# Kernel tuning notes

Hardware: AMD Instinct MI355X
Metric: run time of the kernel (lower is better)

The kernel has to match this reference:

```python
import jax, jax.numpy as jnp
import numpy as np

B, D, H = 8, 512, 8
HD = D // H            # 64 head dim
NS, NT = 8192, 4096    # search / template points
ATTN_EPS = 1e-6
LN_EPS = 1e-5


def layer_norm(x, g, b):
    m = jnp.mean(x, axis=-1, keepdims=True)
    v = jnp.mean((x - m) ** 2, axis=-1, keepdims=True)
    return (x - m) * jax.lax.rsqrt(v + LN_EPS) * g + b


def setup_inputs() -> dict:
    key = jax.random.key(0)
    ks = jax.random.split(key, 20)
    s = 0.02
    return {
        "search_feat": jax.random.normal(ks[0], (B, D, NS), jnp.float32),
        "search_xyz": jax.random.uniform(ks[1], (B, NS, 3), jnp.float32),
        "template_feat": jax.random.normal(ks[2], (B, D, NT), jnp.float32),
        "template_xyz": jax.random.uniform(ks[3], (B, NT, 3), jnp.float32),
        "pos_w1": jax.random.normal(ks[4], (3, D), jnp.float32) * s,
        "pos_b1": jnp.zeros((D,), jnp.float32),
        "pos_w2": jax.random.normal(ks[5], (D, D), jnp.float32) * s,
        "pos_b2": jnp.zeros((D,), jnp.float32),
        "wq": jax.random.normal(ks[6], (D, D), jnp.float32) * s,
        "wk": jax.random.normal(ks[7], (D, D), jnp.float32) * s,
        "wv": jax.random.normal(ks[8], (D, D), jnp.float32) * s,
        "w_merge": jax.random.normal(ks[9], (D, D), jnp.float32) * s,
        "mlp_w1": jax.random.normal(ks[10], (2 * D, 2 * D), jnp.float32) * s,
        "mlp_w2": jax.random.normal(ks[11], (2 * D, D), jnp.float32) * s,
        "ln1_g": jnp.ones((D,), jnp.float32),
        "ln1_b": jnp.zeros((D,), jnp.float32),
        "ln2_g": jnp.ones((D,), jnp.float32),
        "ln2_b": jnp.zeros((D,), jnp.float32),
    }


def reference(search_feat, search_xyz, template_feat, template_xyz,
              pos_w1, pos_b1, pos_w2, pos_b2, wq, wk, wv, w_merge,
              mlp_w1, mlp_w2, ln1_g, ln1_b, ln2_g, ln2_b):
    bs = search_feat.shape[0]
    sf = jnp.transpose(search_feat, (0, 2, 1))    # [B, Ns, D]
    tf = jnp.transpose(template_feat, (0, 2, 1))  # [B, Nt, D]

    # positional MLP on template coordinates
    pos = jax.nn.relu(template_xyz @ pos_w1 + pos_b1) @ pos_w2 + pos_b2
    tf_pos = tf + pos

    q = (sf @ wq).reshape(bs, NS, H, HD)
    k = (tf @ wk).reshape(bs, NT, H, HD)
    v = (tf_pos @ wv).reshape(bs, NT, H, HD)

    # LoFTR-style linear attention: phi(x) = elu(x) + 1
    Q = jax.nn.elu(q) + 1.0
    K = jax.nn.elu(k) + 1.0
    v_len = v.shape[1]
    v_n = v / v_len
    KV = jnp.einsum("bshd,bshv->bhdv", K, v_n)                 # [B,H,d,d]
    Z = 1.0 / (jnp.einsum("blhd,bhd->blh", Q, K.sum(axis=1)) + ATTN_EPS)
    msg = jnp.einsum("blhd,bhdv->blhv", Q, KV) * Z[..., None] * v_len

    msg = msg.reshape(bs, NS, H * HD) @ w_merge
    msg = layer_norm(msg, ln1_g, ln1_b)
    cat = jnp.concatenate([sf, msg], axis=2)                    # [B,Ns,2D]
    msg = jax.nn.relu(cat @ mlp_w1) @ mlp_w2
    msg = layer_norm(msg, ln2_g, ln2_b)
    return jnp.transpose(sf + msg, (0, 2, 1))                   # [B,D,Ns]
```

## Files before the change

kernel.cpp:

```cpp
#include <hip/hip_runtime.h>
#include <stdint.h>
#include <stddef.h>


using ushort_t = unsigned short;
using short8 = __attribute__((ext_vector_type(8))) short;
using f32x4  = __attribute__((ext_vector_type(4))) float;

#define DEVI __device__ __forceinline__

DEVI float b2f(unsigned short u) {
    unsigned v = ((unsigned)u) << 16;
    return __builtin_bit_cast(float, v);
}
DEVI unsigned short f2b(float x) {
    unsigned u = __builtin_bit_cast(unsigned, x);
    u += 0x7FFFu + ((u >> 16) & 1u);
    return (unsigned short)(u >> 16);
}
DEVI void gload16(const void* g, void* l) {
    __builtin_amdgcn_global_load_lds(
        (const __attribute__((address_space(1))) unsigned*)g,
        (__attribute__((address_space(3))) unsigned*)l, 16, 0, 0);
}

template <int EPI>
__global__ __launch_bounds__(512, 2)
void gemm_bf16(const ushort_t* __restrict__ A0, const ushort_t* __restrict__ A1,
               const ushort_t* __restrict__ Wt, ushort_t* __restrict__ C,
               const float* __restrict__ bias, const ushort_t* __restrict__ addm,
               int N, int K, int K0, int lda0, int lda1, int nn)
{
    __shared__ ushort_t As[2][256 * 64];
    __shared__ ushort_t Bs[2][256 * 64];
    const int tid = threadIdx.x;
    const int cpx = gridDim.x >> 3;
    const int lid = (blockIdx.x & 7) * cpx + (blockIdx.x >> 3);
    const int m0 = (lid / nn) * 256;
    const int n0 = (lid % nn) * 256;
    const int w = tid >> 6, l = tid & 63;
    const int wm = (w >> 2) * 128;
    const int wn = (w & 3) * 64;
    const int lr = l & 15, lg = l >> 4;
    const int srow = tid >> 3;
    const int sck  = (tid & 7) ^ (srow & 7);
    const int nk = K / 64;

    f32x4 accA[4][4] = {};
    f32x4 accB[4][4] = {};

    auto stageA = [&](int kt, int buf) {
        const int kb = kt * 64;
        const ushort_t* p; int ld;
        if (kb < K0) { p = A0 + (size_t)m0 * lda0 + kb; ld = lda0; }
        else         { p = A1 + (size_t)m0 * lda1 + (kb - K0); ld = lda1; }
        p += (size_t)srow * ld + sck * 8;
#pragma unroll
        for (int j = 0; j < 4; j++)
            gload16(p + (size_t)(j * 64) * ld,
                    (void*)(&As[buf][j * 4096] + tid * 8));
    };
    auto stageB = [&](int kt, int buf) {
        const ushort_t* p = Wt + (size_t)(n0 + srow) * K + kt * 64 + sck * 8;
#pragma unroll
        for (int j = 0; j < 4; j++)
            gload16(p + (size_t)(j * 64) * K,
                    (void*)(&Bs[buf][j * 4096] + tid * 8));
    };

    short8 aP[4], aQ[4], aR[4], b0[4], b1[4];

    auto ldA = [&](short8 (&dst)[4], int mh, int ks, int cb) {
#pragma unroll
        for (int mf = 0; mf < 4; mf++) {
            const int r = wm + mh * 64 + mf * 16 + lr;
            dst[mf] = *(const short8*)&As[cb][r * 64 + ((ks * 4 + lg) ^ (r & 7)) * 8];
        }
    };
    auto ldB = [&](short8 (&dst)[4], int ks, int cb) {
#pragma unroll
        for (int nf = 0; nf < 4; nf++) {
            const int r = wn + nf * 16 + lr;
            dst[nf] = *(const short8*)&Bs[cb][r * 64 + ((ks * 4 + lg) ^ (r & 7)) * 8];
        }
    };
    auto MM = [&](f32x4 (&ac)[4][4], short8 (&af)[4], short8 (&bf)[4]) {
        __builtin_amdgcn_s_setprio(1);
#pragma unroll
        for (int mf = 0; mf < 4; mf++)
#pragma unroll
            for (int nf = 0; nf < 4; nf++)
                ac[mf][nf] = __builtin_amdgcn_mfma_f32_16x16x32_bf16(
                    af[mf], bf[nf], ac[mf][nf], 0, 0, 0);
        __builtin_amdgcn_s_setprio(0);
    };

    stageA(0, 0); stageB(0, 0);
    asm volatile("s_waitcnt vmcnt(0)" ::: "memory");
    __builtin_amdgcn_s_barrier();
    ldA(aP, 0, 0, 0); ldB(b0, 0, 0);

    for (int t = 0; t < nk; ++t) {
        const int cur = t & 1;
        const bool pre = (t + 1) < nk;
        ldA(aQ, 1, 0, cur); ldB(b1, 1, cur);
        if (pre) stageA(t + 1, cur ^ 1);
        MM(accA, aP, b0);
        ldA(aR, 0, 1, cur);
        if (pre) stageB(t + 1, cur ^ 1);
        MM(accB, aQ, b0);
        ldA(aP, 1, 1, cur);
        MM(accA, aR, b1);
        MM(accB, aP, b1);
        if (pre) {
            asm volatile("s_waitcnt vmcnt(0)" ::: "memory");
            __builtin_amdgcn_s_barrier();
            ldA(aP, 0, 0, cur ^ 1); ldB(b0, 0, cur ^ 1);
        }
    }

#pragma unroll
    for (int mf = 0; mf < 4; mf++) {
#pragma unroll
        for (int i = 0; i < 4; i++) {
            const int mA = m0 + wm + mf * 16 + lg * 4 + i;
            const int mB = mA + 64;
#pragma unroll
            for (int nf = 0; nf < 4; nf++) {
                const int n = n0 + wn + nf * 16 + lr;
                float x = accA[mf][nf][i];
                float y = accB[mf][nf][i];
                if constexpr (EPI == 1) {
                    x = x > 0.f ? x + 1.f : __expf(x);
                    y = y > 0.f ? y + 1.f : __expf(y);
                }
                if constexpr (EPI == 2) {
                    x += bias[n] + b2f(addm[(size_t)mA * N + n]);
                    y += bias[n] + b2f(addm[(size_t)mB * N + n]);
                }
                if constexpr (EPI == 3) { x = fmaxf(x, 0.f); y = fmaxf(y, 0.f); }
                C[(size_t)mA * N + n] = f2b(x);
                C[(size_t)mB * N + n] = f2b(y);
            }
        }
    }
}

__global__ __launch_bounds__(256)
void transpose_f32_bf16(const float* __restrict__ in, ushort_t* __restrict__ out,
                        int R, int Cc)
{
    __shared__ float tile[64][65];
    const int t = threadIdx.x;
    const int c0 = blockIdx.x * 64, r0 = blockIdx.y * 64;
    const size_t bo = (size_t)blockIdx.z * (size_t)R * (size_t)Cc;
    const float* src = in + bo;
    ushort_t* dst = out + bo;
#pragma unroll
    for (int i = 0; i < 4; i++) {
        const int r = (t >> 4) + i * 16;
        const int c = (t & 15) * 4;
        const float4 v = *(const float4*)&src[(size_t)(r0 + r) * Cc + c0 + c];
        tile[r][c + 0] = v.x; tile[r][c + 1] = v.y;
        tile[r][c + 2] = v.z; tile[r][c + 3] = v.w;
    }
    __syncthreads();
#pragma unroll
    for (int i = 0; i < 2; i++) {
        const int c = (t >> 3) + i * 32;
        const int rs = (t & 7) * 8;
        short8 o;
#pragma unroll
        for (int j = 0; j < 8; j++) o[j] = (short)f2b(tile[rs + j][c]);
        *(short8*)&dst[(size_t)(c0 + c) * R + r0 + rs] = o;
    }
}

__global__ __launch_bounds__(256)
void pos_mlp1(const float* __restrict__ xyz, const float* __restrict__ w1,
              const float* __restrict__ b1, ushort_t* __restrict__ P1)
{
    const int t = threadIdx.x;
    const int m = blockIdx.x * 4 + (t >> 6);
    const int n0 = (t & 63) * 8;
    const float x = xyz[m * 3 + 0], y = xyz[m * 3 + 1], z = xyz[m * 3 + 2];
    short8 o;
#pragma unroll
    for (int j = 0; j < 8; j++) {
        const int n = n0 + j;
        float v = x * w1[n] + y * w1[512 + n] + z * w1[1024 + n] + b1[n];
        o[j] = (short)f2b(fmaxf(v, 0.f));
    }
    *(short8*)&P1[(size_t)m * 512 + n0] = o;
}

__global__ __launch_bounds__(256)
void kv_partial(const ushort_t* __restrict__ Kp, const ushort_t* __restrict__ V,
                float* __restrict__ KVp, float* __restrict__ Ksp)
{
    __shared__ ushort_t Ks[256 * 64];
    __shared__ ushort_t Vs[256 * 64];
    const int t = threadIdx.x;
    const int sp = blockIdx.x, h = blockIdx.y, b = blockIdx.z;
    const int d0 = t >> 2, e0 = (t & 3) * 16;
    const int srow = t >> 3, scol = (t & 7) * 8;
    float acc[16] = {};
    float ksum = 0.f;
    for (int c = 0; c < 4; c++) {
        if (c) __syncthreads();
        const size_t sbase = (size_t)b * 4096 + sp * 1024 + c * 256;
#pragma unroll
        for (int i = 0; i < 8; i++) {
            const size_t go = (sbase + i * 32 + srow) * 512 + h * 64 + scol;
            gload16(Kp + go, (void*)(&Ks[i * 2048] + t * 8));
            gload16(V + go, (void*)(&Vs[i * 2048] + t * 8));
        }
        __syncthreads();
        for (int s = 0; s < 256; s++) {
            const float k = b2f(Ks[s * 64 + d0]);
            if ((t & 3) == 0) ksum += k;
            const short8 v0 = *(const short8*)&Vs[s * 64 + e0];
            const short8 v1 = *(const short8*)&Vs[s * 64 + e0 + 8];
#pragma unroll
            for (int j = 0; j < 8; j++) {
                acc[j]     += k * b2f((unsigned short)v0[j]);
                acc[8 + j] += k * b2f((unsigned short)v1[j]);
            }
        }
    }
    const int bh = b * 8 + h;
    float* kvo = KVp + (((size_t)sp * 64 + bh) * 64 + d0) * 64 + e0;
#pragma unroll
    for (int j = 0; j < 16; j++) kvo[j] = acc[j];
    if ((t & 3) == 0) Ksp[((size_t)sp * 64 + bh) * 64 + d0] = ksum;
}

__global__ __launch_bounds__(256)
void kv_finalize(const float* __restrict__ KVp, const float* __restrict__ Ksp,
                 ushort_t* __restrict__ KVt)
{
    const int bh = blockIdx.x, t = threadIdx.x;
    ushort_t* o = KVt + (size_t)bh * 5120;
#pragma unroll
    for (int i = 0; i < 16; i++) {
        const int idx = i * 256 + t;
        const int e = idx >> 6, d = idx & 63;
        float s = 0.f;
#pragma unroll
        for (int sp = 0; sp < 4; sp++)
            s += KVp[(((size_t)sp * 64 + bh) * 64 + d) * 64 + e];
        o[idx] = f2b(s);
    }
    if (t < 64) {
        float s = 0.f;
#pragma unroll
        for (int sp = 0; sp < 4; sp++) s += Ksp[((size_t)sp * 64 + bh) * 64 + t];
        o[4096 + t] = f2b(s);
    }
    for (int idx = 4160 + t; idx < 5120; idx += 256) o[idx] = 0;
}

__global__ __launch_bounds__(256, 2)
void attn_apply(const ushort_t* __restrict__ Qp, const ushort_t* __restrict__ KVt,
                ushort_t* __restrict__ msg1)
{
    __shared__ ushort_t As[256 * 64];
    __shared__ ushort_t Bs[80 * 64];
    const int t = threadIdx.x;
    const int ch = blockIdx.x, h = blockIdx.y, b = blockIdx.z;
    const int w = t >> 6, l = t & 63;
    const int lr = l & 15, lg = l >> 4;
    const int row0 = ch * 256;
    const int srow = t >> 3;
    const int sc = ((t & 7) ^ (srow & 7)) * 8;
    const ushort_t* kv = KVt + (size_t)(b * 8 + h) * 5120;
#pragma unroll
    for (int i = 0; i < 2; i++)
        gload16(kv + (size_t)(i * 32 + srow) * 64 + sc,
                (void*)(&Bs[i * 2048] + t * 8));
    if (t < 128)
        gload16(kv + (size_t)(64 + srow) * 64 + sc,
                (void*)(&Bs[4096] + t * 8));
    const ushort_t* qb = Qp + ((size_t)b * 8192 + row0) * 512 + h * 64;
#pragma unroll
    for (int i = 0; i < 8; i++)
        gload16(qb + (size_t)(i * 32 + srow) * 512 + sc,
                (void*)(&As[i * 2048] + t * 8));
    __syncthreads();
    f32x4 acc[4][5] = {};
    const int wr = w * 64;
#pragma unroll
    for (int ks = 0; ks < 2; ks++) {
        const int kswz = ((ks * 4 + lg) ^ (lr & 7)) * 8;
        short8 a[4], bb[5];
#pragma unroll
        for (int mf = 0; mf < 4; mf++)
            a[mf] = *(const short8*)&As[(wr + mf * 16 + lr) * 64 + kswz];
#pragma unroll
        for (int nf = 0; nf < 5; nf++)
            bb[nf] = *(const short8*)&Bs[(nf * 16 + lr) * 64 + kswz];
#pragma unroll
        for (int mf = 0; mf < 4; mf++)
#pragma unroll
            for (int nf = 0; nf < 5; nf++)
                acc[mf][nf] = __builtin_amdgcn_mfma_f32_16x16x32_bf16(
                    a[mf], bb[nf], acc[mf][nf], 0, 0, 0);
    }
#pragma unroll
    for (int mf = 0; mf < 4; mf++) {
#pragma unroll
        for (int i = 0; i < 4; i++) {
            const int m = row0 + wr + mf * 16 + lg * 4 + i;
            const float zden = __shfl(acc[mf][4][i], (l & 48));
            const float z = 1.f / (zden + 1e-6f);
#pragma unroll
            for (int nf = 0; nf < 4; nf++) {
                const int e = nf * 16 + lr;
                msg1[((size_t)b * 8192 + m) * 512 + h * 64 + e] =
                    f2b(acc[mf][nf][i] * z);
            }
        }
    }
}

__global__ __launch_bounds__(256)
void layer_norm_k(ushort_t* __restrict__ X, const float* __restrict__ g,
                  const float* __restrict__ bta)
{
    const int t = threadIdx.x;
    const int row = blockIdx.x * 4 + (t >> 6);
    const int l = t & 63;
    ushort_t* x = X + (size_t)row * 512;
    const short8 v = *(const short8*)&x[l * 8];
    float f[8];
    float s = 0.f;
#pragma unroll
    for (int j = 0; j < 8; j++) { f[j] = b2f((unsigned short)v[j]); s += f[j]; }
#pragma unroll
    for (int o = 32; o > 0; o >>= 1) s += __shfl_xor(s, o);
    const float mean = s * (1.f / 512.f);
    float vs = 0.f;
#pragma unroll
    for (int j = 0; j < 8; j++) { const float d = f[j] - mean; vs += d * d; }
#pragma unroll
    for (int o = 32; o > 0; o >>= 1) vs += __shfl_xor(vs, o);
    const float rstd = rsqrtf(vs * (1.f / 512.f) + 1e-5f);
    short8 ov;
#pragma unroll
    for (int j = 0; j < 8; j++) {
        const int c = l * 8 + j;
        ov[j] = (short)f2b((f[j] - mean) * rstd * g[c] + bta[c]);
    }
    *(short8*)&x[l * 8] = ov;
}

__global__ __launch_bounds__(256)
void ln2_final(const ushort_t* __restrict__ outp, const ushort_t* __restrict__ sfT,
               const float* __restrict__ g, const float* __restrict__ bta,
               float* __restrict__ out)
{
    __shared__ ushort_t tile[64][514];
    const int t = threadIdx.x;
    const int ns0 = blockIdx.x * 64, b = blockIdx.y;
    const int w = t >> 6, l = t & 63;
#pragma unroll
    for (int rr = 0; rr < 16; rr++) {
        const int r = w * 16 + rr;
        const size_t grow = (size_t)b * 8192 + ns0 + r;
        const short8 v = *(const short8*)&outp[grow * 512 + l * 8];
        float f[8];
        float s = 0.f;
#pragma unroll
        for (int j = 0; j < 8; j++) { f[j] = b2f((unsigned short)v[j]); s += f[j]; }
#pragma unroll
        for (int o = 32; o > 0; o >>= 1) s += __shfl_xor(s, o);
        const float mean = s * (1.f / 512.f);
        float vs = 0.f;
#pragma unroll
        for (int j = 0; j < 8; j++) { const float d = f[j] - mean; vs += d * d; }
#pragma unroll
        for (int o = 32; o > 0; o >>= 1) vs += __shfl_xor(vs, o);
        const float rstd = rsqrtf(vs * (1.f / 512.f) + 1e-5f);
        const short8 sv = *(const short8*)&sfT[grow * 512 + l * 8];
        short8 ov;
#pragma unroll
        for (int j = 0; j < 8; j++) {
            const int c = l * 8 + j;
            ov[j] = (short)f2b(b2f((unsigned short)sv[j]) +
                               (f[j] - mean) * rstd * g[c] + bta[c]);
        }
        *(short8*)&tile[r][l * 8] = ov;
    }
    __syncthreads();
#pragma unroll
    for (int i = 0; i < 32; i++) {
        const int d = (t >> 4) + i * 16;
        const int nss = (t & 15) * 4;
        float4 o;
        o.x = b2f(tile[nss + 0][d]);
        o.y = b2f(tile[nss + 1][d]);
        o.z = b2f(tile[nss + 2][d]);
        o.w = b2f(tile[nss + 3][d]);
        *(float4*)&out[((size_t)b * 512 + d) * 8192 + ns0 + nss] = o;
    }
}

extern "C" void kernel_launch(void* const* d_in, const int* in_sizes, int n_in,
                              void* d_out, int out_size, void* d_ws, size_t ws_size,
                              hipStream_t stream)
{
    (void)in_sizes; (void)n_in; (void)out_size; (void)ws_size;
    const float* search_feat   = (const float*)d_in[0];
    const float* template_feat = (const float*)d_in[2];
    const float* template_xyz  = (const float*)d_in[3];
    const float* pos_w1  = (const float*)d_in[4];
    const float* pos_b1  = (const float*)d_in[5];
    const float* pos_w2  = (const float*)d_in[6];
    const float* pos_b2  = (const float*)d_in[7];
    const float* wq      = (const float*)d_in[8];
    const float* wk      = (const float*)d_in[9];
    const float* wv      = (const float*)d_in[10];
    const float* w_merge = (const float*)d_in[11];
    const float* mlp_w1  = (const float*)d_in[12];
    const float* mlp_w2  = (const float*)d_in[13];
    const float* ln1_g   = (const float*)d_in[14];
    const float* ln1_b   = (const float*)d_in[15];
    const float* ln2_g   = (const float*)d_in[16];
    const float* ln2_b   = (const float*)d_in[17];
    float* out = (float*)d_out;

    char* ws = (char*)d_ws;
    ushort_t* sfT    = (ushort_t*)(ws + 0);
    ushort_t* Qp     = (ushort_t*)(ws + 67108864);
    ushort_t* tfT    = (ushort_t*)(ws + 134217728);
    ushort_t* Kp     = (ushort_t*)(ws + 167772160);
    ushort_t* msg2   = (ushort_t*)(ws + 134217728);
    ushort_t* P1     = (ushort_t*)(ws + 201326592);
    ushort_t* Vv     = (ushort_t*)(ws + 201326592);
    ushort_t* tfpos  = (ushort_t*)(ws + 234881024);
    ushort_t* msg1   = (ushort_t*)(ws + 268435456);
    ushort_t* hidden = (ushort_t*)(ws + 201326592);
    ushort_t* outp   = Qp;
    ushort_t* wqT  = (ushort_t*)(ws + 335544320);
    ushort_t* wkT  = (ushort_t*)(ws + 336068608);
    ushort_t* wvT  = (ushort_t*)(ws + 336592896);
    ushort_t* wmT  = (ushort_t*)(ws + 337117184);
    ushort_t* pw2T = (ushort_t*)(ws + 337641472);
    ushort_t* w1T  = (ushort_t*)(ws + 338165760);
    ushort_t* w2T  = (ushort_t*)(ws + 340262912);
    float*    KVp  = (float*)(ws + 341311488);
    float*    Ksp  = (float*)(ws + 345505792);
    ushort_t* KVt  = (ushort_t*)(ws + 345571328);

    transpose_f32_bf16<<<dim3(128, 8, 8), 256, 0, stream>>>(search_feat, sfT, 512, 8192);
    transpose_f32_bf16<<<dim3(64, 8, 8), 256, 0, stream>>>(template_feat, tfT, 512, 4096);
    transpose_f32_bf16<<<dim3(8, 8, 1), 256, 0, stream>>>(wq, wqT, 512, 512);
    transpose_f32_bf16<<<dim3(8, 8, 1), 256, 0, stream>>>(wk, wkT, 512, 512);
    transpose_f32_bf16<<<dim3(8, 8, 1), 256, 0, stream>>>(wv, wvT, 512, 512);
    transpose_f32_bf16<<<dim3(8, 8, 1), 256, 0, stream>>>(w_merge, wmT, 512, 512);
    transpose_f32_bf16<<<dim3(8, 8, 1), 256, 0, stream>>>(pos_w2, pw2T, 512, 512);
    transpose_f32_bf16<<<dim3(16, 16, 1), 256, 0, stream>>>(mlp_w1, w1T, 1024, 1024);
    transpose_f32_bf16<<<dim3(8, 16, 1), 256, 0, stream>>>(mlp_w2, w2T, 1024, 512);

    gemm_bf16<1><<<dim3(512), 512, 0, stream>>>(sfT, nullptr, wqT, Qp,
                                                nullptr, nullptr, 512, 512, 512, 512, 0, 2);
    gemm_bf16<1><<<dim3(256), 512, 0, stream>>>(tfT, nullptr, wkT, Kp,
                                                nullptr, nullptr, 512, 512, 512, 512, 0, 2);
    pos_mlp1<<<dim3(8192), 256, 0, stream>>>(template_xyz, pos_w1, pos_b1, P1);
    gemm_bf16<2><<<dim3(256), 512, 0, stream>>>(P1, nullptr, pw2T, tfpos,
                                                pos_b2, tfT, 512, 512, 512, 512, 0, 2);
    gemm_bf16<0><<<dim3(256), 512, 0, stream>>>(tfpos, nullptr, wvT, Vv,
                                                nullptr, nullptr, 512, 512, 512, 512, 0, 2);
    kv_partial<<<dim3(4, 8, 8), 256, 0, stream>>>(Kp, Vv, KVp, Ksp);
    kv_finalize<<<dim3(64), 256, 0, stream>>>(KVp, Ksp, KVt);
    attn_apply<<<dim3(32, 8, 8), 256, 0, stream>>>(Qp, KVt, msg1);
    gemm_bf16<0><<<dim3(512), 512, 0, stream>>>(msg1, nullptr, wmT, msg2,
                                                nullptr, nullptr, 512, 512, 512, 512, 0, 2);
    layer_norm_k<<<dim3(16384), 256, 0, stream>>>(msg2, ln1_g, ln1_b);
    gemm_bf16<3><<<dim3(1024), 512, 0, stream>>>(sfT, msg2, w1T, hidden,
                                                 nullptr, nullptr, 1024, 1024, 512, 512, 512, 4);
    gemm_bf16<0><<<dim3(512), 512, 0, stream>>>(hidden, nullptr, w2T, outp,
                                                nullptr, nullptr, 512, 1024, 1024, 1024, 0, 2);
    ln2_final<<<dim3(128, 8), 256, 0, stream>>>(outp, sfT, ln2_g, ln2_b, out);
}
```

Measured before the change: 707.1 us.

## Merge prep transposes and pos-MLP into one launch; batch Q and K GEMMs

```diff
diff --git a/kernel.cpp b/kernel.cpp
--- a/kernel.cpp
+++ b/kernel.cpp
@@ -146,16 +146,172 @@
     }
 }
 
+__global__ __launch_bounds__(512, 2)
+void gemm_qk(const ushort_t* __restrict__ sfT, const ushort_t* __restrict__ tfT,
+             const ushort_t* __restrict__ wqT, const ushort_t* __restrict__ wkT,
+             ushort_t* __restrict__ Qp, ushort_t* __restrict__ Kp)
+{
+    __shared__ ushort_t As[2][256 * 64];
+    __shared__ ushort_t Bs[2][256 * 64];
+    const int tid = threadIdx.x;
+    const int cpx = gridDim.x >> 3;
+    const int lid = (blockIdx.x & 7) * cpx + (blockIdx.x >> 3);
+    const ushort_t* A0; const ushort_t* Wt; ushort_t* C; int loc;
+    if (lid < 512) { loc = lid;       A0 = sfT; Wt = wqT; C = Qp; }
+    else           { loc = lid - 512; A0 = tfT; Wt = wkT; C = Kp; }
+    const int m0 = (loc >> 1) * 256;
+    const int n0 = (loc & 1) * 256;
+    const int w = tid >> 6, l = tid & 63;
+    const int wm = (w >> 2) * 128;
+    const int wn = (w & 3) * 64;
+    const int lr = l & 15, lg = l >> 4;
+    const int srow = tid >> 3;
+    const int sck  = (tid & 7) ^ (srow & 7);
+    const int nk = 8;
+
+    f32x4 accA[4][4] = {};
+    f32x4 accB[4][4] = {};
+
+    auto stageA = [&](int kt, int buf) {
+        const ushort_t* p = A0 + (size_t)(m0 + srow) * 512 + kt * 64 + sck * 8;
+#pragma unroll
+        for (int j = 0; j < 4; j++)
+            gload16(p + (size_t)(j * 64) * 512,
+                    (void*)(&As[buf][j * 4096] + tid * 8));
+    };
+    auto stageB = [&](int kt, int buf) {
+        const ushort_t* p = Wt + (size_t)(n0 + srow) * 512 + kt * 64 + sck * 8;
+#pragma unroll
+        for (int j = 0; j < 4; j++)
+            gload16(p + (size_t)(j * 64) * 512,
+                    (void*)(&Bs[buf][j * 4096] + tid * 8));
+    };
+
+    short8 aP[4], aQ[4], aR[4], b0[4], b1[4];
+
+    auto ldA = [&](short8 (&dst)[4], int mh, int ks, int cb) {
+#pragma unroll
+        for (int mf = 0; mf < 4; mf++) {
+            const int r = wm + mh * 64 + mf * 16 + lr;
+            dst[mf] = *(const short8*)&As[cb][r * 64 + ((ks * 4 + lg) ^ (r & 7)) * 8];
+        }
+    };
+    auto ldB = [&](short8 (&dst)[4], int ks, int cb) {
+#pragma unroll
+        for (int nf = 0; nf < 4; nf++) {
+            const int r = wn + nf * 16 + lr;
+            dst[nf] = *(const short8*)&Bs[cb][r * 64 + ((ks * 4 + lg) ^ (r & 7)) * 8];
+        }
+    };
+    auto MM = [&](f32x4 (&ac)[4][4], short8 (&af)[4], short8 (&bf)[4]) {
+        __builtin_amdgcn_s_setprio(1);
+#pragma unroll
+        for (int mf = 0; mf < 4; mf++)
+#pragma unroll
+            for (int nf = 0; nf < 4; nf++)
+                ac[mf][nf] = __builtin_amdgcn_mfma_f32_16x16x32_bf16(
+                    af[mf], bf[nf], ac[mf][nf], 0, 0, 0);
+        __builtin_amdgcn_s_setprio(0);
+    };
+
+    stageA(0, 0); stageB(0, 0);
+    asm volatile("s_waitcnt vmcnt(0)" ::: "memory");
+    __builtin_amdgcn_s_barrier();
+    ldA(aP, 0, 0, 0); ldB(b0, 0, 0);
+
+    for (int t = 0; t < nk; ++t) {
+        const int cur = t & 1;
+        const bool pre = (t + 1) < nk;
+        ldA(aQ, 1, 0, cur); ldB(b1, 1, cur);
+        if (pre) stageA(t + 1, cur ^ 1);
+        MM(accA, aP, b0);
+        ldA(aR, 0, 1, cur);
+        if (pre) stageB(t + 1, cur ^ 1);
+        MM(accB, aQ, b0);
+        ldA(aP, 1, 1, cur);
+        MM(accA, aR, b1);
+        MM(accB, aP, b1);
+        if (pre) {
+            asm volatile("s_waitcnt vmcnt(0)" ::: "memory");
+            __builtin_amdgcn_s_barrier();
+            ldA(aP, 0, 0, cur ^ 1); ldB(b0, 0, cur ^ 1);
+        }
+    }
+
+#pragma unroll
+    for (int mf = 0; mf < 4; mf++) {
+#pragma unroll
+        for (int i = 0; i < 4; i++) {
+            const int mA = m0 + wm + mf * 16 + lg * 4 + i;
+            const int mB = mA + 64;
+#pragma unroll
+            for (int nf = 0; nf < 4; nf++) {
+                const int n = n0 + wn + nf * 16 + lr;
+                float x = accA[mf][nf][i];
+                float y = accB[mf][nf][i];
+                x = x > 0.f ? x + 1.f : __expf(x);
+                y = y > 0.f ? y + 1.f : __expf(y);
+                C[(size_t)mA * 512 + n] = f2b(x);
+                C[(size_t)mB * 512 + n] = f2b(y);
+            }
+        }
+    }
+}
+
 __global__ __launch_bounds__(256)
-void transpose_f32_bf16(const float* __restrict__ in, ushort_t* __restrict__ out,
-                        int R, int Cc)
-{
+void prep(const float* __restrict__ sfeat, const float* __restrict__ tfeat,
+          const float* __restrict__ xyz, const float* __restrict__ pw1,
+          const float* __restrict__ pb1,
+          const float* wq, const float* wk, const float* wv, const float* wm,
+          const float* pw2, const float* w1, const float* w2,
+          ushort_t* sfT, ushort_t* tfT, ushort_t* P1,
+          ushort_t* wqT, ushort_t* wkT, ushort_t* wvT, ushort_t* wmT,
+          ushort_t* pw2T, ushort_t* w1T, ushort_t* w2T)
+{
+    const int bid = blockIdx.x;
+    const int t = threadIdx.x;
+    if (bid >= 12992) {
+        const int m = (bid - 12992) * 4 + (t >> 6);
+        const int n0 = (t & 63) * 8;
+        const float x = xyz[m * 3 + 0], y = xyz[m * 3 + 1], z = xyz[m * 3 + 2];
+        short8 o;
+#pragma unroll
+        for (int j = 0; j < 8; j++) {
+            const int n = n0 + j;
+            float v = x * pw1[n] + y * pw1[512 + n] + z * pw1[1024 + n] + pb1[n];
+            o[j] = (short)f2b(fmaxf(v, 0.f));
+        }
+        *(short8*)&P1[(size_t)m * 512 + n0] = o;
+        return;
+    }
     __shared__ float tile[64][65];
-    const int t = threadIdx.x;
-    const int c0 = blockIdx.x * 64, r0 = blockIdx.y * 64;
-    const size_t bo = (size_t)blockIdx.z * (size_t)R * (size_t)Cc;
-    const float* src = in + bo;
-    ushort_t* dst = out + bo;
+    const float* src; ushort_t* dst; int R, Cc, c0, r0;
+    if (bid < 8192) {
+        const int b = bid >> 10, rem = bid & 1023;
+        src = sfeat + (size_t)b * 512 * 8192; dst = sfT + (size_t)b * 512 * 8192;
+        R = 512; Cc = 8192; c0 = (rem & 127) * 64; r0 = (rem >> 7) * 64;
+    } else if (bid < 12288) {
+        const int lcl = bid - 8192; const int b = lcl >> 9, rem = lcl & 511;
+        src = tfeat + (size_t)b * 512 * 4096; dst = tfT + (size_t)b * 512 * 4096;
+        R = 512; Cc = 4096; c0 = (rem & 63) * 64; r0 = (rem >> 6) * 64;
+    } else {
+        const int lcl = bid - 12288;
+        if (lcl < 320) {
+            const int wsel = lcl >> 6, local = lcl & 63;
+            const float* srcs[5] = {wq, wk, wv, wm, pw2};
+            ushort_t* dsts[5] = {wqT, wkT, wvT, wmT, pw2T};
+            src = srcs[wsel]; dst = dsts[wsel];
+            R = 512; Cc = 512; c0 = (local & 7) * 64; r0 = (local >> 3) * 64;
+        } else if (lcl < 576) {
+            const int local = lcl - 320;
+            src = w1; dst = w1T; R = 1024; Cc = 1024;
+            c0 = (local & 15) * 64; r0 = (local >> 4) * 64;
+        } else {
+            const int local = lcl - 576;
+            src = w2; dst = w2T; R = 1024; Cc = 512;
+            c0 = (local & 7) * 64; r0 = (local >> 3) * 64;
+        }
+    }
 #pragma unroll
     for (int i = 0; i < 4; i++) {
         const int r = (t >> 4) + i * 16;
@@ -174,24 +330,6 @@
         for (int j = 0; j < 8; j++) o[j] = (short)f2b(tile[rs + j][c]);
         *(short8*)&dst[(size_t)(c0 + c) * R + r0 + rs] = o;
     }
-}
-
-__global__ __launch_bounds__(256)
-void pos_mlp1(const float* __restrict__ xyz, const float* __restrict__ w1,
-              const float* __restrict__ b1, ushort_t* __restrict__ P1)
-{
-    const int t = threadIdx.x;
-    const int m = blockIdx.x * 4 + (t >> 6);
-    const int n0 = (t & 63) * 8;
-    const float x = xyz[m * 3 + 0], y = xyz[m * 3 + 1], z = xyz[m * 3 + 2];
-    short8 o;
-#pragma unroll
-    for (int j = 0; j < 8; j++) {
-        const int n = n0 + j;
-        float v = x * w1[n] + y * w1[512 + n] + z * w1[1024 + n] + b1[n];
-        o[j] = (short)f2b(fmaxf(v, 0.f));
-    }
-    *(short8*)&P1[(size_t)m * 512 + n0] = o;
 }
 
 __global__ __launch_bounds__(256)
@@ -452,21 +590,11 @@
     float*    Ksp  = (float*)(ws + 345505792);
     ushort_t* KVt  = (ushort_t*)(ws + 345571328);
 
-    transpose_f32_bf16<<<dim3(128, 8, 8), 256, 0, stream>>>(search_feat, sfT, 512, 8192);
-    transpose_f32_bf16<<<dim3(64, 8, 8), 256, 0, stream>>>(template_feat, tfT, 512, 4096);
-    transpose_f32_bf16<<<dim3(8, 8, 1), 256, 0, stream>>>(wq, wqT, 512, 512);
-    transpose_f32_bf16<<<dim3(8, 8, 1), 256, 0, stream>>>(wk, wkT, 512, 512);
-    transpose_f32_bf16<<<dim3(8, 8, 1), 256, 0, stream>>>(wv, wvT, 512, 512);
-    transpose_f32_bf16<<<dim3(8, 8, 1), 256, 0, stream>>>(w_merge, wmT, 512, 512);
-    transpose_f32_bf16<<<dim3(8, 8, 1), 256, 0, stream>>>(pos_w2, pw2T, 512, 512);
-    transpose_f32_bf16<<<dim3(16, 16, 1), 256, 0, stream>>>(mlp_w1, w1T, 1024, 1024);
-    transpose_f32_bf16<<<dim3(8, 16, 1), 256, 0, stream>>>(mlp_w2, w2T, 1024, 512);
-
-    gemm_bf16<1><<<dim3(512), 512, 0, stream>>>(sfT, nullptr, wqT, Qp,
-                                                nullptr, nullptr, 512, 512, 512, 512, 0, 2);
-    gemm_bf16<1><<<dim3(256), 512, 0, stream>>>(tfT, nullptr, wkT, Kp,
-                                                nullptr, nullptr, 512, 512, 512, 512, 0, 2);
-    pos_mlp1<<<dim3(8192), 256, 0, stream>>>(template_xyz, pos_w1, pos_b1, P1);
+    prep<<<dim3(21184), 256, 0, stream>>>(
+        search_feat, template_feat, template_xyz, pos_w1, pos_b1,
+        wq, wk, wv, w_merge, pos_w2, mlp_w1, mlp_w2,
+        sfT, tfT, P1, wqT, wkT, wvT, wmT, pw2T, w1T, w2T);
+    gemm_qk<<<dim3(768), 512, 0, stream>>>(sfT, tfT, wqT, wkT, Qp, Kp);
     gemm_bf16<2><<<dim3(256), 512, 0, stream>>>(P1, nullptr, pw2T, tfpos,
                                                 pos_b2, tfT, 512, 512, 512, 512, 0, 2);
     gemm_bf16<0><<<dim3(256), 512, 0, stream>>>(tfpos, nullptr, wvT, Vv,
```

New measurement: 701.8 us. Within noise of the previous version (-0.8%).
